# Performance work log

Measured on AMD Instinct MI355X. Metric: run time of the kernel, lower is better.

The kernel has to match this reference:

```python
import jax, jax.numpy as jnp
import numpy as np

B, N, E, H, TOP_K = 2, 2048, 1024, 16, 64
Dh = E // H


def _linear_init(k, fan_in, shape):
    bound = 1.0 / np.sqrt(fan_in)
    return jax.random.uniform(k, shape, jnp.float32, -bound, bound)


def setup_inputs() -> dict:
    key = jax.random.key(0)
    ks = jax.random.split(key, 11)
    return {
        "query": jax.random.normal(ks[0], (B, N, E), jnp.float32),
        "key": jax.random.normal(ks[1], (B, N, E), jnp.float32),
        "value": jax.random.normal(ks[2], (B, N, E), jnp.float32),
        "Wq": _linear_init(ks[3], E, (E, E)),
        "bq": _linear_init(ks[4], E, (E,)),
        "Wk": _linear_init(ks[5], E, (E, E)),
        "bk": _linear_init(ks[6], E, (E,)),
        "Wv": _linear_init(ks[7], E, (E, E)),
        "bv": _linear_init(ks[8], E, (E,)),
        "Wo": _linear_init(ks[9], E, (E, E)),
        "bo": _linear_init(ks[10], E, (E,)),
    }


def _split_heads(x):
    # (B, N, E) -> (B*H, N, Dh)
    return x.reshape(B, N, H, Dh).transpose(0, 2, 1, 3).reshape(B * H, N, Dh)


def _merge_heads(x):
    # (B*H, N, Dh) -> (B, N, E)
    return x.reshape(B, H, N, Dh).transpose(0, 2, 1, 3).reshape(B, N, E)


def _topk_attention(q, k, v, top_k):
    # q,k,v: (BH, N, Dh). Faithful to _classical_efficient_attention:
    # scores scaled by sqrt(last dim of Q) == sqrt(Dh).
    scores = jnp.einsum("bqd,bkd->bqk", q, k) / jnp.sqrt(jnp.float32(q.shape[-1]))
    top_scores, top_idx = jax.lax.top_k(scores, min(top_k, scores.shape[-1]))
    w = jax.nn.softmax(top_scores, axis=-1)  # (BH, Nq, K)
    # gather V rows: (BH, 1, Nk, Dh) indexed along axis 2 -> (BH, Nq, K, Dh)
    vals = jnp.take_along_axis(v[:, None, :, :], top_idx[..., None], axis=2)
    return jnp.einsum("bqk,bqkd->bqd", w, vals)


def reference(query, key, value, Wq, bq, Wk, bk, Wv, bv, Wo, bo):
    q = _split_heads(query @ Wq.T + bq)
    k = _split_heads(key @ Wk.T + bk)
    v = _split_heads(value @ Wv.T + bv)
    out = _topk_attention(q, k, v, TOP_K)
    return _merge_heads(out) @ Wo.T + bo
```

## Files before the change

kernel.cpp:

```cpp
#include <hip/hip_runtime.h>
#include <stdint.h>
#include <math.h>

#define Bk 2
#define Nk 2048
#define Ek 1024
#define Hk 16
#define DHk 64
#define BLENDW 5e-5
#define PRECAND 96
#define CANDCAP 128

using short8 = __attribute__((ext_vector_type(8))) short;
using f32x4  = __attribute__((ext_vector_type(4))) float;

__device__ __forceinline__ unsigned short bf16rne(float f) {
    const unsigned u = __float_as_uint(f);
    return (unsigned short)((u + 0x7FFFu + ((u >> 16) & 1u)) >> 16);
}

__global__ __launch_bounds__(256) void cvt_split(
    const float* __restrict__ in, unsigned short* __restrict__ oh,
    unsigned short* __restrict__ ol)
{
    const int i = blockIdx.x * 256 + threadIdx.x;
    const float4 a = ((const float4*)in)[i * 2];
    const float4 b = ((const float4*)in)[i * 2 + 1];
    float x[8] = {a.x, a.y, a.z, a.w, b.x, b.y, b.z, b.w};
    unsigned short hs[8], ls[8];
#pragma unroll
    for (int j = 0; j < 8; ++j) {
        hs[j] = bf16rne(x[j]);
        const float hf = __uint_as_float((unsigned)hs[j] << 16);
        ls[j] = bf16rne(x[j] - hf);
    }
    uint4 ho, lo;
    ho.x = hs[0] | ((unsigned)hs[1] << 16); ho.y = hs[2] | ((unsigned)hs[3] << 16);
    ho.z = hs[4] | ((unsigned)hs[5] << 16); ho.w = hs[6] | ((unsigned)hs[7] << 16);
    lo.x = ls[0] | ((unsigned)ls[1] << 16); lo.y = ls[2] | ((unsigned)ls[3] << 16);
    lo.z = ls[4] | ((unsigned)ls[5] << 16); lo.w = ls[6] | ((unsigned)ls[7] << 16);
    ((uint4*)oh)[i] = ho;
    ((uint4*)ol)[i] = lo;
}

template<int MODE>
__global__ __launch_bounds__(256, 4) void gemm_mfma(
    const unsigned short* __restrict__ Xh, const unsigned short* __restrict__ Xl,
    const unsigned short* __restrict__ Wh, const unsigned short* __restrict__ Wl,
    const float* __restrict__ bias, float* __restrict__ out,
    unsigned short* __restrict__ obf)
{
    __shared__ unsigned short Ah[128][40], Al[128][40];
    __shared__ unsigned short Bh[64][40],  Bl[64][40];

    const int tid  = threadIdx.x;
    const int lane = tid & 63;
    const int wv   = tid >> 6;
    const int n16  = lane & 15;
    const int quad = lane >> 4;
    const int mBase = blockIdx.y * 128;
    const int nBase = blockIdx.x * 64;

    f32x4 acc[2][4];
#pragma unroll
    for (int i = 0; i < 2; ++i)
#pragma unroll
        for (int j = 0; j < 4; ++j) acc[i][j] = (f32x4){0.f, 0.f, 0.f, 0.f};

    const int arow = tid >> 1, aoff = (tid & 1) * 16;
    const int brow = tid >> 2, boff = (tid & 3) * 8;
    const size_t aIdx = (size_t)(mBase + arow) * Ek + aoff;
    const size_t bIdx = (size_t)(nBase + brow) * Ek + boff;

    for (int kt = 0; kt < Ek; kt += 32) {
        const uint4 ah0 = *(const uint4*)(Xh + aIdx + kt);
        const uint4 ah1 = *(const uint4*)(Xh + aIdx + kt + 8);
        const uint4 al0 = *(const uint4*)(Xl + aIdx + kt);
        const uint4 al1 = *(const uint4*)(Xl + aIdx + kt + 8);
        const uint4 bh0 = *(const uint4*)(Wh + bIdx + kt);
        const uint4 bl0 = *(const uint4*)(Wl + bIdx + kt);
        __syncthreads();
        *(uint4*)&Ah[arow][aoff]     = ah0;
        *(uint4*)&Ah[arow][aoff + 8] = ah1;
        *(uint4*)&Al[arow][aoff]     = al0;
        *(uint4*)&Al[arow][aoff + 8] = al1;
        *(uint4*)&Bh[brow][boff]     = bh0;
        *(uint4*)&Bl[brow][boff]     = bl0;
        __syncthreads();

        const short8 fa_h0 = *(const short8*)&Ah[wv*32 +      n16][quad*8];
        const short8 fa_l0 = *(const short8*)&Al[wv*32 +      n16][quad*8];
        const short8 fa_h1 = *(const short8*)&Ah[wv*32 + 16 + n16][quad*8];
        const short8 fa_l1 = *(const short8*)&Al[wv*32 + 16 + n16][quad*8];
#pragma unroll
        for (int ct = 0; ct < 4; ++ct) {
            const short8 fb_h = *(const short8*)&Bh[ct*16 + n16][quad*8];
            const short8 fb_l = *(const short8*)&Bl[ct*16 + n16][quad*8];
            acc[0][ct] = __builtin_amdgcn_mfma_f32_16x16x32_bf16(fa_h0, fb_h, acc[0][ct], 0, 0, 0);
            acc[0][ct] = __builtin_amdgcn_mfma_f32_16x16x32_bf16(fa_h0, fb_l, acc[0][ct], 0, 0, 0);
            acc[0][ct] = __builtin_amdgcn_mfma_f32_16x16x32_bf16(fa_l0, fb_h, acc[0][ct], 0, 0, 0);
            acc[1][ct] = __builtin_amdgcn_mfma_f32_16x16x32_bf16(fa_h1, fb_h, acc[1][ct], 0, 0, 0);
            acc[1][ct] = __builtin_amdgcn_mfma_f32_16x16x32_bf16(fa_h1, fb_l, acc[1][ct], 0, 0, 0);
            acc[1][ct] = __builtin_amdgcn_mfma_f32_16x16x32_bf16(fa_l1, fb_h, acc[1][ct], 0, 0, 0);
        }
    }

#pragma unroll
    for (int mt = 0; mt < 2; ++mt)
#pragma unroll
    for (int ct = 0; ct < 4; ++ct) {
        const int c  = nBase + ct*16 + n16;
        const float bv = bias[c];
#pragma unroll
        for (int reg = 0; reg < 4; ++reg) {
            const int m = mBase + wv*32 + mt*16 + quad*4 + reg;
            const float o = acc[mt][ct][reg] + bv;
            if (MODE == 0) {
                out[(size_t)m * Ek + c] = o;
            } else {
                const int bb2 = m >> 11, nn = m & 2047;
                const int hh2 = c >> 6,  dd = c & 63;
                const size_t sb = (size_t)(bb2*Hk + hh2) * Nk * DHk;
                out[sb + (size_t)nn * DHk + dd] = o;
                if (obf) {
                    const size_t kdst = sb + (size_t)(nn >> 4) * 1024
                                      + ((dd >> 5) * 512)
                                      + ((((dd >> 3) & 3) * 16 + (nn & 15)) * 8)
                                      + (dd & 7);
                    obf[kdst] = bf16rne(o);
                }
            }
        }
    }
}

__device__ __forceinline__ unsigned fkey(float s) {
    const unsigned b = __float_as_uint(s);
    return (b & 0x80000000u) ? ~b : (b | 0x80000000u);
}
__device__ __forceinline__ unsigned long long dkey(double s) {
    unsigned long long b = (unsigned long long)__double_as_longlong(s);
    return (b & 0x8000000000000000ull) ? ~b : (b | 0x8000000000000000ull);
}
__device__ __forceinline__ double dinv(unsigned long long u) {
    const unsigned long long b =
        (u & 0x8000000000000000ull) ? (u & 0x7fffffffffffffffull) : ~u;
    return __longlong_as_double((long long)b);
}

__device__ __forceinline__ int dpp_wsum_i32(int x) {
#define STEP(C) x += __builtin_amdgcn_update_dpp(0, x, C, 0xf, 0xf, true);
    STEP(0x111) STEP(0x112) STEP(0x114) STEP(0x118) STEP(0x142) STEP(0x143)
#undef STEP
    return __builtin_amdgcn_readlane(x, 63);
}
__device__ __forceinline__ float dpp_wsum_f32(float x) {
#define STEP(C) { const int t_ = __builtin_amdgcn_update_dpp(0, __float_as_int(x), C, 0xf, 0xf, true); \
                  x += __int_as_float(t_); }
    STEP(0x111) STEP(0x112) STEP(0x114) STEP(0x118) STEP(0x142) STEP(0x143)
#undef STEP
    return __int_as_float(__builtin_amdgcn_readlane(__float_as_int(x), 63));
}
__device__ __forceinline__ float dpp_wmax_f32(float x) {
#define STEP(C) { const int t_ = __builtin_amdgcn_update_dpp(__float_as_int(x), __float_as_int(x), C, 0xf, 0xf, false); \
                  x = fmaxf(x, __int_as_float(t_)); }
    STEP(0x111) STEP(0x112) STEP(0x114) STEP(0x118) STEP(0x142) STEP(0x143)
#undef STEP
    return __int_as_float(__builtin_amdgcn_readlane(__float_as_int(x), 63));
}
__device__ __forceinline__ unsigned dpp_wmin_u32(unsigned x) {
#define STEP(C) { const unsigned t_ = (unsigned)__builtin_amdgcn_update_dpp((int)x, (int)x, C, 0xf, 0xf, false); \
                  x = x < t_ ? x : t_; }
    STEP(0x111) STEP(0x112) STEP(0x114) STEP(0x118) STEP(0x142) STEP(0x143)
#undef STEP
    return (unsigned)__builtin_amdgcn_readlane((int)x, 63);
}
__device__ __forceinline__ unsigned dpp_wmax_u32(unsigned x) {
#define STEP(C) { const unsigned t_ = (unsigned)__builtin_amdgcn_update_dpp((int)x, (int)x, C, 0xf, 0xf, false); \
                  x = x > t_ ? x : t_; }
    STEP(0x111) STEP(0x112) STEP(0x114) STEP(0x118) STEP(0x142) STEP(0x143)
#undef STEP
    return (unsigned)__builtin_amdgcn_readlane((int)x, 63);
}
__device__ __forceinline__ int dpp_wprefix_incl_i32(int x) {
    x += __builtin_amdgcn_update_dpp(0, x, 0x111, 0xf, 0xf, true);
    x += __builtin_amdgcn_update_dpp(0, x, 0x112, 0xf, 0xf, true);
    x += __builtin_amdgcn_update_dpp(0, x, 0x114, 0xf, 0xf, true);
    x += __builtin_amdgcn_update_dpp(0, x, 0x118, 0xf, 0xf, true);
    x += __builtin_amdgcn_update_dpp(0, x, 0x142, 0xa, 0xf, true);
    x += __builtin_amdgcn_update_dpp(0, x, 0x143, 0xc, 0xf, true);
    return x;
}

__device__ __forceinline__ void proc_row(
    const int lane, const int lrow,
    unsigned s0, unsigned s1, unsigned s2, unsigned s3,
    unsigned s4, unsigned s5, unsigned s6, unsigned s7,
    unsigned s8, unsigned s9, unsigned s10, unsigned s11,
    unsigned s12, unsigned s13, unsigned s14, unsigned s15,
    const float* __restrict__ Kb, const float (*qsf)[68],
    unsigned long long (*ck)[CANDCAP], unsigned (*ci)[CANDCAP],
    unsigned long long (*wvi)[64], unsigned (*eq_idx)[64],
    int& i65_out, float& lam_out)
{
    const unsigned long long lmask = (1ull << lane) - 1ull;

    const unsigned q0 = s0 << 16,  q1 = s1 << 16,  q2 = s2 << 16,  q3 = s3 << 16;
    const unsigned q4 = s4 << 16,  q5 = s5 << 16,  q6 = s6 << 16,  q7 = s7 << 16;
    const unsigned q8 = s8 << 16,  q9 = s9 << 16,  q10 = s10 << 16, q11 = s11 << 16;
    const unsigned q12 = s12 << 16, q13 = s13 << 16, q14 = s14 << 16, q15 = s15 << 16;

    unsigned m1 = 0u, m2 = 0u;
#define T2(V) { const unsigned t_ = (V) < m1 ? (V) : m1; \
                m1 = m1 > (V) ? m1 : (V);  m2 = m2 > t_ ? m2 : t_; }
    T2(s0)  T2(s1)  T2(s2)  T2(s3)  T2(s4)  T2(s5)  T2(s6)  T2(s7)
    T2(s8)  T2(s9)  T2(s10) T2(s11) T2(s12) T2(s13) T2(s14) T2(s15)
    T2(q0)  T2(q1)  T2(q2)  T2(q3)  T2(q4)  T2(q5)  T2(q6)  T2(q7)
    T2(q8)  T2(q9)  T2(q10) T2(q11) T2(q12) T2(q13) T2(q14) T2(q15)
#undef T2
    unsigned lo16 = dpp_wmin_u32(m2) >> 16;
    unsigned hi16 = dpp_wmax_u32(m1) >> 16;

    while (lo16 < hi16) {
        const unsigned mid = lo16 + ((hi16 - lo16) >> 1) + 1u;
        const unsigned M = mid << 16;
        int c0 = 0, c1 = 0, c2 = 0, c3 = 0;
        c0 += (s0  >= M); c0 += (q0  >= M); c0 += (s1  >= M); c0 += (q1  >= M);
        c0 += (s2  >= M); c0 += (q2  >= M); c0 += (s3  >= M); c0 += (q3  >= M);
        c1 += (s4  >= M); c1 += (q4  >= M); c1 += (s5  >= M); c1 += (q5  >= M);
        c1 += (s6  >= M); c1 += (q6  >= M); c1 += (s7  >= M); c1 += (q7  >= M);
        c2 += (s8  >= M); c2 += (q8  >= M); c2 += (s9  >= M); c2 += (q9  >= M);
        c2 += (s10 >= M); c2 += (q10 >= M); c2 += (s11 >= M); c2 += (q11 >= M);
        c3 += (s12 >= M); c3 += (q12 >= M); c3 += (s13 >= M); c3 += (q13 >= M);
        c3 += (s14 >= M); c3 += (q14 >= M); c3 += (s15 >= M); c3 += (q15 >= M);
        const int c = dpp_wsum_i32((c0 + c1) + (c2 + c3));
        if (c >= PRECAND) {
            lo16 = mid;
            if (c <= CANDCAP) break;
        } else hi16 = mid - 1u;
    }
    const unsigned THsh = lo16 << 16;

    int cnt = 0;
#define CC(S, Q) { cnt += ((Q) >= THsh); cnt += ((S) >= THsh); }
    CC(s0, q0)    CC(s1, q1)    CC(s2, q2)    CC(s3, q3)
    CC(s4, q4)    CC(s5, q5)    CC(s6, q6)    CC(s7, q7)
    CC(s8, q8)    CC(s9, q9)    CC(s10, q10)  CC(s11, q11)
    CC(s12, q12)  CC(s13, q13)  CC(s14, q14)  CC(s15, q15)
#undef CC
    const int incl = dpp_wprefix_incl_i32(cnt);
    int pos = incl - cnt;
    int nc = __builtin_amdgcn_readlane(incl, 63);
    if (nc > CANDCAP) nc = CANDCAP;
#define CE(W, S, Q) { \
        if ((Q) >= THsh) { \
            if (pos < CANDCAP) \
                ci[lrow][pos] = (unsigned)((((W) >> 2) * 512) + (((W) & 3) * 128) + 2 * lane); \
            ++pos; } \
        if ((S) >= THsh) { \
            if (pos < CANDCAP) \
                ci[lrow][pos] = (unsigned)((((W) >> 2) * 512) + (((W) & 3) * 128) + 2 * lane + 1); \
            ++pos; } }
    CE(0, s0, q0)     CE(1, s1, q1)     CE(2, s2, q2)     CE(3, s3, q3)
    CE(4, s4, q4)     CE(5, s5, q5)     CE(6, s6, q6)     CE(7, s7, q7)
    CE(8, s8, q8)     CE(9, s9, q9)     CE(10, s10, q10)  CE(11, s11, q11)
    CE(12, s12, q12)  CE(13, s13, q13)  CE(14, s14, q14)  CE(15, s15, q15)
#undef CE

    const int c8 = lane >> 3, d8 = lane & 7;
    const float* qrow = &qsf[lrow][d8 * 8];
    const double qd0 = (double)qrow[0], qd1 = (double)qrow[1];
    const double qd2 = (double)qrow[2], qd3 = (double)qrow[3];
    const double qd4 = (double)qrow[4], qd5 = (double)qrow[5];
    const double qd6 = (double)qrow[6], qd7 = (double)qrow[7];
    const int nb = (nc + 7) >> 3;
    for (int b = 0; b < nb; ++b) {
        const int s  = b * 8 + c8;
        const int s2 = s < nc ? s : nc - 1;
        const unsigned cidx = ci[lrow][s2];
        const unsigned kb32 = (cidx << 6) + (unsigned)(d8 * 8);
        const float2 kv0 = *(const float2*)(Kb + kb32);
        const float2 kv1 = *(const float2*)(Kb + kb32 + 2);
        const float2 kv2 = *(const float2*)(Kb + kb32 + 4);
        const float2 kv3 = *(const float2*)(Kb + kb32 + 6);
        double acc = 0.0;
        acc = fma(qd0, (double)kv0.x, acc);
        acc = fma(qd1, (double)kv0.y, acc);
        acc = fma(qd2, (double)kv1.x, acc);
        acc = fma(qd3, (double)kv1.y, acc);
        acc = fma(qd4, (double)kv2.x, acc);
        acc = fma(qd5, (double)kv2.y, acc);
        acc = fma(qd6, (double)kv3.x, acc);
        acc = fma(qd7, (double)kv3.y, acc);
        acc += __shfl_xor(acc, 1);
        acc += __shfl_xor(acc, 2);
        acc += __shfl_xor(acc, 4);
        if (d8 == 0 && s < nc) ck[lrow][s] = dkey(acc * 0.125);
    }

    const unsigned long long k0 = (lane      < nc) ? ck[lrow][lane]      : 0ull;
    const unsigned long long k1 = (lane + 64 < nc) ? ck[lrow][lane + 64] : 0ull;
    const unsigned idx0 = ci[lrow][lane];
    const unsigned idx1 = ci[lrow][(lane + 64) & (CANDCAP - 1)];
    const unsigned kh0 = (unsigned)(k0 >> 32), kh1 = (unsigned)(k1 >> 32);
    const unsigned kl0 = (unsigned)k0,         kl1 = (unsigned)k1;

    unsigned H;
    {
        const unsigned i0 = (k0 != 0ull) ? kh0 : 0xFFFFFFFFu;
        const unsigned i1 = (k1 != 0ull) ? kh1 : 0xFFFFFFFFu;
        unsigned lo = dpp_wmin_u32(i0 < i1 ? i0 : i1);
        unsigned hi = dpp_wmax_u32(kh0 > kh1 ? kh0 : kh1);
        bool done = false;
        while (lo < hi) {
            const unsigned mid = lo + ((hi - lo) >> 1) + 1u;
            const int c = __popcll(__ballot(kh0 >= mid))
                        + __popcll(__ballot(kh1 >= mid));
            if (c == 64) {
                const unsigned v0 = (kh0 >= mid) ? kh0 : 0xFFFFFFFFu;
                const unsigned v1m = (kh1 >= mid) ? kh1 : 0xFFFFFFFFu;
                H = dpp_wmin_u32(v0 < v1m ? v0 : v1m);
                done = true; break;
            }
            if (c >= 64) lo = mid; else hi = mid - 1u;
        }
        if (!done) H = lo;
    }
    const int cGtHi = __popcll(__ballot(kh0 > H))
                    + __popcll(__ballot(kh1 > H));
    const int need1 = 64 - cGtHi;

    const bool e0v = (kh0 == H) && (k0 != 0ull);
    const bool e1v = (kh1 == H) && (k1 != 0ull);
    const int cEq = __popcll(__ballot(e0v)) + __popcll(__ballot(e1v));
    unsigned Tlo;
    if (need1 == cEq) {
        const unsigned v0 = e0v ? kl0 : 0xFFFFFFFFu;
        const unsigned v1m = e1v ? kl1 : 0xFFFFFFFFu;
        Tlo = dpp_wmin_u32(v0 < v1m ? v0 : v1m);
    } else if (need1 == 1) {
        const unsigned v0 = e0v ? kl0 : 0u;
        const unsigned v1m = e1v ? kl1 : 0u;
        Tlo = dpp_wmax_u32(v0 > v1m ? v0 : v1m);
    } else {
        unsigned lo = 0u, hi = 0xFFFFFFFFu;
        bool done = false;
        while (lo < hi) {
            const unsigned mid = lo + ((hi - lo) >> 1) + 1u;
            const int c = __popcll(__ballot(e0v && kl0 >= mid))
                        + __popcll(__ballot(e1v && kl1 >= mid));
            if (c == need1) {
                const unsigned v0 = (e0v && kl0 >= mid) ? kl0 : 0xFFFFFFFFu;
                const unsigned v1m = (e1v && kl1 >= mid) ? kl1 : 0xFFFFFFFFu;
                Tlo = dpp_wmin_u32(v0 < v1m ? v0 : v1m);
                done = true; break;
            }
            if (c >= need1) lo = mid; else hi = mid - 1u;
        }
        if (!done) Tlo = lo;
    }
    const unsigned long long T = ((unsigned long long)H << 32) | Tlo;

    int base = 0;
    {
        const bool g0 = k0 > T;
        unsigned long long m = __ballot(g0);
        if (g0) {
            const int pos2 = base + __popcll(m & lmask);
            wvi[lrow][pos2] = ((unsigned long long)__float_as_uint((float)dinv(k0)) << 32)
                            | (unsigned long long)idx0;
        }
        base += __popcll(m);
        const bool g1 = k1 > T;
        m = __ballot(g1);
        if (g1) {
            const int pos2 = base + __popcll(m & lmask);
            wvi[lrow][pos2] = ((unsigned long long)__float_as_uint((float)dinv(k1)) << 32)
                            | (unsigned long long)idx1;
        }
        base += __popcll(m);
    }

    int ne = 0;
    {
        const bool e0 = k0 == T;
        unsigned long long m = __ballot(e0);
        if (e0) {
            const int pos2 = ne + __popcll(m & lmask);
            if (pos2 < 64) eq_idx[lrow][pos2] = idx0;
        }
        ne += __popcll(m);
        const bool e1 = k1 == T;
        m = __ballot(e1);
        if (e1) {
            const int pos2 = ne + __popcll(m & lmask);
            if (pos2 < 64) eq_idx[lrow][pos2] = idx1;
        }
        ne += __popcll(m);
    }
    if (ne > 64) ne = 64;

    const int   need = 64 - base;
    const float tvf  = (float)dinv(T);
    if (lane < need) {
        unsigned my = 0u;
        for (int j = 0; j < ne; ++j) {
            const unsigned v = eq_idx[lrow][j];
            int rank = 0;
            for (int j2 = 0; j2 < ne; ++j2) rank += (eq_idx[lrow][j2] < v) ? 1 : 0;
            if (rank == lane) my = v;
        }
        wvi[lrow][base + lane] = ((unsigned long long)__float_as_uint(tvf) << 32)
                               | (unsigned long long)my;
    }

    const unsigned mh0 = (k0 < T) ? kh0 : 0u;
    const unsigned mh1 = (k1 < T) ? kh1 : 0u;
    const unsigned Hm = dpp_wmax_u32(mh0 > mh1 ? mh0 : mh1);
    const unsigned ml0 = (k0 < T && kh0 == Hm) ? kl0 : 0u;
    const unsigned ml1 = (k1 < T && kh1 == Hm) ? kl1 : 0u;
    const unsigned Lm = dpp_wmax_u32(ml0 > ml1 ? ml0 : ml1);
    const unsigned long long m2k = ((unsigned long long)Hm << 32) | Lm;

    int i65 = 0;
    {
        unsigned long long mm = __ballot(k0 == m2k && m2k != 0ull);
        if (mm) i65 = __shfl((int)idx0, (int)(__ffsll((long long)mm) - 1));
        else {
            mm = __ballot(k1 == m2k && m2k != 0ull);
            if (mm) i65 = __shfl((int)idx1, (int)(__ffsll((long long)mm) - 1));
        }
    }
    double fr = (dinv(T) - dinv(m2k)) * (1.0 / BLENDW);
    if (fr > 1.0) fr = 1.0;
    i65_out = i65;
    lam_out = (m2k == 0ull) ? 0.f : (float)(0.5 * (1.0 - fr));
}

__global__ __launch_bounds__(1024, 8) void attn_topk_mfma(
    const float* __restrict__ qf, const float* __restrict__ kf,
    const unsigned short* __restrict__ kbf,
    const float* __restrict__ vh, float* __restrict__ outm)
{
    __shared__ __align__(16) char uS[33024];
    float (*sc)[516] = (float(*)[516])uS;
    unsigned long long (*ck)[CANDCAP] = (unsigned long long(*)[CANDCAP])uS;
    unsigned (*ci)[CANDCAP] = (unsigned(*)[CANDCAP])(uS + 16384);

    __shared__ float          qsf[16][68];
    __shared__ unsigned short qbf[16][72];
    __shared__ unsigned long long wvi[16][64];
    __shared__ unsigned eq_idx[16][64];

    const int tid  = threadIdx.x;
    const int lane = tid & 63;
    const int wv   = tid >> 6;

    const int wid  = (blockIdx.x & 7) * 512 + (blockIdx.x >> 3);
    const int slot = wid >> 7;
    const int qt   = wid & 127;
    const int bb   = slot >> 4;
    const int hh   = slot & 15;

    const float*          Qb = qf  + (size_t)slot * Nk * DHk + (size_t)qt * 16 * DHk;
    const float*          Kb = kf  + (size_t)slot * Nk * DHk;
    const unsigned short* KB = kbf + (size_t)slot * Nk * DHk;
    const float*          Vb = vh  + (size_t)slot * Nk * DHk;

    {
        const int r = tid >> 6, d = tid & 63;
        const float qv = Qb[r * DHk + d];
        qsf[r][d] = qv;
        qbf[r][d] = bf16rne(qv);
    }
    __syncthreads();

    const int n16  = lane & 15;
    const int quad = lane >> 4;
    short8 afrag0, afrag1;
    afrag0 = *(const short8*)&qbf[n16][quad * 8];
    afrag1 = *(const short8*)&qbf[n16][32 + quad * 8];

    unsigned p0, p1, p2, p3, p4, p5, p6, p7;
    unsigned p8, p9, p10, p11, p12, p13, p14, p15;
    const int rowD = quad * 4;

#define QK_TILE(CH, T, ACC) { \
    const unsigned short* kp = KB + (((CH) * 32) + (wv * 2 + (T))) * 1024 + lane * 8; \
    const short8 b0_ = *(const short8*)(kp); \
    const short8 b1_ = *(const short8*)(kp + 512); \
    ACC = __builtin_amdgcn_mfma_f32_16x16x32_bf16(afrag0, b0_, ACC, 0, 0, 0); \
    ACC = __builtin_amdgcn_mfma_f32_16x16x32_bf16(afrag1, b1_, ACC, 0, 0, 0); \
}
#define SC_STORE(T, ACC) { \
    const int ccol = (wv * 2 + (T)) * 16 + n16; \
    sc[rowD + 0][ccol] = ACC[0]; sc[rowD + 1][ccol] = ACC[1]; \
    sc[rowD + 2][ccol] = ACC[2]; sc[rowD + 3][ccol] = ACC[3]; \
}
#define PACKW(J, DEST) { \
    const float2 pr_ = *(const float2*)&sc[wv][(J) * 128 + 2 * lane]; \
    DEST = (fkey(pr_.x) >> 16) | ((fkey(pr_.y) >> 16) << 16); \
}
#define DO_CHUNK(CH, D0, D1, D2, D3) { \
    f32x4 ac0 = {0.f,0.f,0.f,0.f}, ac1 = {0.f,0.f,0.f,0.f}; \
    QK_TILE(CH, 0, ac0) QK_TILE(CH, 1, ac1) \
    __syncthreads();                    \
    SC_STORE(0, ac0) SC_STORE(1, ac1) \
    __syncthreads(); \
    PACKW(0, D0) PACKW(1, D1) PACKW(2, D2) PACKW(3, D3) \
}
    DO_CHUNK(0, p0,  p1,  p2,  p3)
    DO_CHUNK(1, p4,  p5,  p6,  p7)
    DO_CHUNK(2, p8,  p9,  p10, p11)
    DO_CHUNK(3, p12, p13, p14, p15)
#undef DO_CHUNK
#undef PACKW
#undef SC_STORE
#undef QK_TILE

    __syncthreads();

    int i65_0; float lam_0;
    proc_row(lane, wv,
             p0, p1, p2, p3, p4, p5, p6, p7,
             p8, p9, p10, p11, p12, p13, p14, p15,
             Kb, qsf, ck, ci, wvi, eq_idx, i65_0, lam_0);

    {
        const unsigned long long e = wvi[wv][lane];
        const float    sv = __uint_as_float((unsigned)(e >> 32));
        const unsigned vi = (unsigned)e;
        const float mx = dpp_wmax_f32(sv);
        const float p  = __expf(sv - mx);
        const float Z  = dpp_wsum_f32(p);
        const float w  = p / Z;
        wvi[wv][lane] = ((unsigned long long)__float_as_uint(w) << 32)
                      | (unsigned long long)vi;

        float acc = 0.f;
#pragma unroll
        for (int j = 0; j < 64; ++j) {
            const unsigned long long ej = wvi[wv][j];
            const float wj = __uint_as_float((unsigned)(ej >> 32));
            const unsigned ij = (unsigned)ej;
            acc = fmaf(wj, Vb[(ij << 6) + (unsigned)lane], acc);
        }
        {
            const unsigned long long e63 = wvi[wv][63];
            const float    wT  = __uint_as_float((unsigned)(e63 >> 32));
            const unsigned i64 = (unsigned)e63;
            acc += wT * lam_0 *
                   (Vb[((unsigned)i65_0 << 6) + (unsigned)lane]
                  - Vb[(i64 << 6) + (unsigned)lane]);
        }
        const int gq = qt * 16 + wv;
        outm[((size_t)bb * Nk + gq) * Ek + hh * DHk + lane] = acc;
    }
}

extern "C" void kernel_launch(void* const* d_in, const int* in_sizes, int n_in,
                              void* d_out, int out_size, void* d_ws, size_t ws_size,
                              hipStream_t stream)
{
    const float* query = (const float*)d_in[0];
    const float* key   = (const float*)d_in[1];
    const float* value = (const float*)d_in[2];
    const float* Wq    = (const float*)d_in[3];
    const float* bq    = (const float*)d_in[4];
    const float* Wk    = (const float*)d_in[5];
    const float* bk    = (const float*)d_in[6];
    const float* Wv    = (const float*)d_in[7];
    const float* bv    = (const float*)d_in[8];
    const float* Wo    = (const float*)d_in[9];
    const float* bo    = (const float*)d_in[10];
    float* out = (float*)d_out;
    (void)in_sizes; (void)n_in; (void)out_size; (void)ws_size;

    const size_t seg  = (size_t)(Bk * Hk) * Nk * DHk;
    const size_t wseg = (size_t)Ek * Ek;
    float* qfp = (float*)d_ws;
    float* kfp = qfp + seg;
    float* vws = kfp + seg;
    float* aws = vws + seg;
    unsigned short* kbf = (unsigned short*)(aws + seg);
    unsigned short* xh  = kbf + seg;
    unsigned short* xl  = xh + seg;
    unsigned short* wh  = xl + seg;
    unsigned short* wl  = wh + wseg;

    const dim3 blk(256);
    const dim3 gG(16, 32);
    const int  gX = (int)(seg  / 2048);
    const int  gW = (int)(wseg / 2048);

    hipLaunchKernelGGL(cvt_split, dim3(gX), blk, 0, stream, query, xh, xl);
    hipLaunchKernelGGL(cvt_split, dim3(gW), blk, 0, stream, Wq, wh, wl);
    hipLaunchKernelGGL((gemm_mfma<1>), gG, blk, 0, stream, xh, xl, wh, wl, bq, qfp, (unsigned short*)nullptr);
    hipLaunchKernelGGL(cvt_split, dim3(gX), blk, 0, stream, key, xh, xl);
    hipLaunchKernelGGL(cvt_split, dim3(gW), blk, 0, stream, Wk, wh, wl);
    hipLaunchKernelGGL((gemm_mfma<1>), gG, blk, 0, stream, xh, xl, wh, wl, bk, kfp, kbf);
    hipLaunchKernelGGL(cvt_split, dim3(gX), blk, 0, stream, value, xh, xl);
    hipLaunchKernelGGL(cvt_split, dim3(gW), blk, 0, stream, Wv, wh, wl);
    hipLaunchKernelGGL((gemm_mfma<1>), gG, blk, 0, stream, xh, xl, wh, wl, bv, vws, (unsigned short*)nullptr);
    hipLaunchKernelGGL(attn_topk_mfma, dim3(32 * 128), dim3(1024), 0, stream,
                       qfp, kfp, kbf, vws, aws);
    hipLaunchKernelGGL(cvt_split, dim3(gX), blk, 0, stream, aws, xh, xl);
    hipLaunchKernelGGL(cvt_split, dim3(gW), blk, 0, stream, Wo, wh, wl);
    hipLaunchKernelGGL((gemm_mfma<0>), gG, blk, 0, stream, xh, xl, wh, wl, bo, out, (unsigned short*)nullptr);
}
```

Before: 560.0 us.

## Fuse activation split-conversion into GEMM and batch QKV projections in one launch

Activation fp32→bf16 hi/lo splitting moves into the GEMM A-tile load, so the separate conversion kernels and their workspace round trips go away. All four weight matrices are converted in a single launch, and the Q/K/V projections run as one grid of 1536 blocks. Block indices are remapped so the XCDs get interleaved work. In exchange, each GEMM block re-converts its A tile once for every N tile, which adds ALU work and reads fp32 activations (twice the bytes of bf16) repeatedly.

```diff
diff --git a/kernel.cpp b/kernel.cpp
--- a/kernel.cpp
+++ b/kernel.cpp
@@ -19,36 +19,54 @@
     return (unsigned short)((u + 0x7FFFu + ((u >> 16) & 1u)) >> 16);
 }
 
-__global__ __launch_bounds__(256) void cvt_split(
-    const float* __restrict__ in, unsigned short* __restrict__ oh,
-    unsigned short* __restrict__ ol)
+__device__ __forceinline__ void cvt8hl(const float4 a, const float4 b,
+                                       uint4& ho, uint4& lo) {
+    const unsigned short h0 = bf16rne(a.x), h1 = bf16rne(a.y);
+    const unsigned short h2 = bf16rne(a.z), h3 = bf16rne(a.w);
+    const unsigned short h4 = bf16rne(b.x), h5 = bf16rne(b.y);
+    const unsigned short h6 = bf16rne(b.z), h7 = bf16rne(b.w);
+    const unsigned short l0 = bf16rne(a.x - __uint_as_float((unsigned)h0 << 16));
+    const unsigned short l1 = bf16rne(a.y - __uint_as_float((unsigned)h1 << 16));
+    const unsigned short l2 = bf16rne(a.z - __uint_as_float((unsigned)h2 << 16));
+    const unsigned short l3 = bf16rne(a.w - __uint_as_float((unsigned)h3 << 16));
+    const unsigned short l4 = bf16rne(b.x - __uint_as_float((unsigned)h4 << 16));
+    const unsigned short l5 = bf16rne(b.y - __uint_as_float((unsigned)h5 << 16));
+    const unsigned short l6 = bf16rne(b.z - __uint_as_float((unsigned)h6 << 16));
+    const unsigned short l7 = bf16rne(b.w - __uint_as_float((unsigned)h7 << 16));
+    ho.x = h0 | ((unsigned)h1 << 16); ho.y = h2 | ((unsigned)h3 << 16);
+    ho.z = h4 | ((unsigned)h5 << 16); ho.w = h6 | ((unsigned)h7 << 16);
+    lo.x = l0 | ((unsigned)l1 << 16); lo.y = l2 | ((unsigned)l3 << 16);
+    lo.z = l4 | ((unsigned)l5 << 16); lo.w = l6 | ((unsigned)l7 << 16);
+}
+
+__global__ __launch_bounds__(256) void cvt_w(
+    const float* __restrict__ W0, const float* __restrict__ W1,
+    const float* __restrict__ W2, const float* __restrict__ W3,
+    unsigned short* __restrict__ whb, unsigned short* __restrict__ wlb)
 {
-    const int i = blockIdx.x * 256 + threadIdx.x;
+    const int seg = blockIdx.x >> 9;
+    const int loc = blockIdx.x & 511;
+    const float* in = (seg == 0) ? W0 : (seg == 1) ? W1 : (seg == 2) ? W2 : W3;
+    unsigned short* oh = whb + (size_t)seg * Ek * Ek;
+    unsigned short* ol = wlb + (size_t)seg * Ek * Ek;
+    const int i = loc * 256 + threadIdx.x;
     const float4 a = ((const float4*)in)[i * 2];
-    const float4 b = ((const float4*)in)[i * 2 + 1];
-    float x[8] = {a.x, a.y, a.z, a.w, b.x, b.y, b.z, b.w};
-    unsigned short hs[8], ls[8];
-#pragma unroll
-    for (int j = 0; j < 8; ++j) {
-        hs[j] = bf16rne(x[j]);
-        const float hf = __uint_as_float((unsigned)hs[j] << 16);
-        ls[j] = bf16rne(x[j] - hf);
-    }
+    const float4 c = ((const float4*)in)[i * 2 + 1];
     uint4 ho, lo;
-    ho.x = hs[0] | ((unsigned)hs[1] << 16); ho.y = hs[2] | ((unsigned)hs[3] << 16);
-    ho.z = hs[4] | ((unsigned)hs[5] << 16); ho.w = hs[6] | ((unsigned)hs[7] << 16);
-    lo.x = ls[0] | ((unsigned)ls[1] << 16); lo.y = ls[2] | ((unsigned)ls[3] << 16);
-    lo.z = ls[4] | ((unsigned)ls[5] << 16); lo.w = ls[6] | ((unsigned)ls[7] << 16);
+    cvt8hl(a, c, ho, lo);
     ((uint4*)oh)[i] = ho;
     ((uint4*)ol)[i] = lo;
 }
 
 template<int MODE>
 __global__ __launch_bounds__(256, 4) void gemm_mfma(
-    const unsigned short* __restrict__ Xh, const unsigned short* __restrict__ Xl,
-    const unsigned short* __restrict__ Wh, const unsigned short* __restrict__ Wl,
-    const float* __restrict__ bias, float* __restrict__ out,
-    unsigned short* __restrict__ obf)
+    const float* __restrict__ X0, const float* __restrict__ X1,
+    const float* __restrict__ X2,
+    const unsigned short* __restrict__ whb, const unsigned short* __restrict__ wlb,
+    const float* __restrict__ b0, const float* __restrict__ b1,
+    const float* __restrict__ b2,
+    float* __restrict__ o0, float* __restrict__ o1, float* __restrict__ o2,
+    unsigned short* __restrict__ kbf)
 {
     __shared__ unsigned short Ah[128][40], Al[128][40];
     __shared__ unsigned short Bh[64][40],  Bl[64][40];
@@ -58,8 +76,25 @@
     const int wv   = tid >> 6;
     const int n16  = lane & 15;
     const int quad = lane >> 4;
-    const int mBase = blockIdx.y * 128;
-    const int nBase = blockIdx.x * 64;
+
+    int proj, loc;
+    if (MODE == 1) {
+        const int wid = (blockIdx.x & 7) * 192 + (blockIdx.x >> 3);
+        proj = wid >> 9;
+        loc  = wid & 511;
+    } else {
+        proj = 0;
+        loc  = (blockIdx.x & 7) * 64 + (blockIdx.x >> 3);
+    }
+    const int mBase = (loc >> 4) * 128;
+    const int nBase = (loc & 15) * 64;
+
+    const float* X    = (proj == 0) ? X0 : (proj == 1) ? X1 : X2;
+    const float* bias = (proj == 0) ? b0 : (proj == 1) ? b1 : b2;
+    float*       out  = (proj == 0) ? o0 : (proj == 1) ? o1 : o2;
+    unsigned short* obf = (MODE == 1 && proj == 1) ? kbf : (unsigned short*)nullptr;
+    const unsigned short* Wh = whb + (size_t)proj * Ek * Ek;
+    const unsigned short* Wl = wlb + (size_t)proj * Ek * Ek;
 
     f32x4 acc[2][4];
 #pragma unroll
@@ -73,12 +108,15 @@
     const size_t bIdx = (size_t)(nBase + brow) * Ek + boff;
 
     for (int kt = 0; kt < Ek; kt += 32) {
-        const uint4 ah0 = *(const uint4*)(Xh + aIdx + kt);
-        const uint4 ah1 = *(const uint4*)(Xh + aIdx + kt + 8);
-        const uint4 al0 = *(const uint4*)(Xl + aIdx + kt);
-        const uint4 al1 = *(const uint4*)(Xl + aIdx + kt + 8);
+        const float4 x0 = *(const float4*)(X + aIdx + kt);
+        const float4 x1 = *(const float4*)(X + aIdx + kt + 4);
+        const float4 x2 = *(const float4*)(X + aIdx + kt + 8);
+        const float4 x3 = *(const float4*)(X + aIdx + kt + 12);
         const uint4 bh0 = *(const uint4*)(Wh + bIdx + kt);
         const uint4 bl0 = *(const uint4*)(Wl + bIdx + kt);
+        uint4 ah0, al0, ah1, al1;
+        cvt8hl(x0, x1, ah0, al0);
+        cvt8hl(x2, x3, ah1, al1);
         __syncthreads();
         *(uint4*)&Ah[arow][aoff]     = ah0;
         *(uint4*)&Ah[arow][aoff + 8] = ah1;
@@ -583,28 +621,22 @@
     float* vws = kfp + seg;
     float* aws = vws + seg;
     unsigned short* kbf = (unsigned short*)(aws + seg);
-    unsigned short* xh  = kbf + seg;
-    unsigned short* xl  = xh + seg;
-    unsigned short* wh  = xl + seg;
-    unsigned short* wl  = wh + wseg;
+    unsigned short* whb = kbf + seg;
+    unsigned short* wlb = whb + 4 * wseg;
 
     const dim3 blk(256);
-    const dim3 gG(16, 32);
-    const int  gX = (int)(seg  / 2048);
-    const int  gW = (int)(wseg / 2048);
-
-    hipLaunchKernelGGL(cvt_split, dim3(gX), blk, 0, stream, query, xh, xl);
-    hipLaunchKernelGGL(cvt_split, dim3(gW), blk, 0, stream, Wq, wh, wl);
-    hipLaunchKernelGGL((gemm_mfma<1>), gG, blk, 0, stream, xh, xl, wh, wl, bq, qfp, (unsigned short*)nullptr);
-    hipLaunchKernelGGL(cvt_split, dim3(gX), blk, 0, stream, key, xh, xl);
-    hipLaunchKernelGGL(cvt_split, dim3(gW), blk, 0, stream, Wk, wh, wl);
-    hipLaunchKernelGGL((gemm_mfma<1>), gG, blk, 0, stream, xh, xl, wh, wl, bk, kfp, kbf);
-    hipLaunchKernelGGL(cvt_split, dim3(gX), blk, 0, stream, value, xh, xl);
-    hipLaunchKernelGGL(cvt_split, dim3(gW), blk, 0, stream, Wv, wh, wl);
-    hipLaunchKernelGGL((gemm_mfma<1>), gG, blk, 0, stream, xh, xl, wh, wl, bv, vws, (unsigned short*)nullptr);
+
+    hipLaunchKernelGGL(cvt_w, dim3(4 * 512), blk, 0, stream,
+                       Wq, Wk, Wv, Wo, whb, wlb);
+    hipLaunchKernelGGL((gemm_mfma<1>), dim3(3 * 512), blk, 0, stream,
+                       query, key, value, whb, wlb, bq, bk, bv,
+                       qfp, kfp, vws, kbf);
     hipLaunchKernelGGL(attn_topk_mfma, dim3(32 * 128), dim3(1024), 0, stream,
                        qfp, kfp, kbf, vws, aws);
-    hipLaunchKernelGGL(cvt_split, dim3(gX), blk, 0, stream, aws, xh, xl);
-    hipLaunchKernelGGL(cvt_split, dim3(gW), blk, 0, stream, Wo, wh, wl);
-    hipLaunchKernelGGL((gemm_mfma<0>), gG, blk, 0, stream, xh, xl, wh, wl, bo, out, (unsigned short*)nullptr);
-}
+    hipLaunchKernelGGL((gemm_mfma<0>), dim3(512), blk, 0, stream,
+                       aws, (const float*)nullptr, (const float*)nullptr,
+                       whb + 3 * wseg, wlb + 3 * wseg,
+                       bo, (const float*)nullptr, (const float*)nullptr,
+                       out, (float*)nullptr, (float*)nullptr,
+                       (unsigned short*)nullptr);
+}
```

Measured after the change: 521.2 us. -6.9%, faster.
